# Performance work log

Hardware: AMD Instinct MI355X
Metric: run time of the kernel (lower is better)

Reference implementation:

```python
import jax, jax.numpy as jnp
import numpy as np

N = 100000   # nodes
E = 1600000  # edges
IN = 128
HID = 128    # 2 * out_channels
OUT = 64


def setup_inputs() -> dict:
    key = jax.random.key(0)
    ks = jax.random.split(key, 8)
    x = jax.random.normal(ks[0], (N, IN), dtype=jnp.float32)
    edge_index = jax.random.randint(ks[1], (2, E), 0, N, dtype=jnp.int32)
    s = 1.0 / np.sqrt(IN)
    W1 = jax.random.normal(ks[2], (IN, HID), dtype=jnp.float32) * s
    Wm1 = jax.random.normal(ks[3], (HID, HID), dtype=jnp.float32) * s
    Wm2 = jax.random.normal(ks[4], (HID, HID), dtype=jnp.float32) * s
    W2 = jax.random.normal(ks[5], (HID, OUT), dtype=jnp.float32) * s
    b1 = jnp.zeros((HID,), jnp.float32)
    bm1 = jnp.zeros((HID,), jnp.float32)
    bm2 = jnp.zeros((HID,), jnp.float32)
    b2 = jnp.zeros((OUT,), jnp.float32)
    return {"x": x, "edge_index": edge_index, "W1": W1, "b1": b1,
            "Wm1": Wm1, "bm1": bm1, "Wm2": Wm2, "bm2": bm2,
            "W2": W2, "b2": b2}


def _gcn_norm(edge_index, num_nodes):
    # PyG GCNConv: add self-loops (weight 1), symmetric normalization.
    loop = jnp.arange(num_nodes, dtype=edge_index.dtype)
    src = jnp.concatenate([edge_index[0], loop])
    dst = jnp.concatenate([edge_index[1], loop])
    deg = jax.ops.segment_sum(jnp.ones_like(src, jnp.float32), dst,
                              num_segments=num_nodes)
    dinv = jnp.where(deg > 0, jax.lax.rsqrt(deg), 0.0)
    norm = dinv[src] * dinv[dst]  # [E + N]
    return src, dst, norm


def _gcn_conv(h, W, b, src, dst, norm, num_nodes):
    h = h @ W                                # dense transform [N, F_out]
    msg = h[src] * norm[:, None]             # gather + scale   [E+N, F_out]
    out = jax.ops.segment_sum(msg, dst, num_segments=num_nodes)  # scatter-add
    return out + b


def reference(x, edge_index, W1, b1, Wm1, bm1, Wm2, bm2, W2, b2):
    num_nodes = x.shape[0]
    src, dst, norm = _gcn_norm(edge_index, num_nodes)
    h = jax.nn.relu(_gcn_conv(x, W1, b1, src, dst, norm, num_nodes))
    h = jax.nn.relu(_gcn_conv(h, Wm1, bm1, src, dst, norm, num_nodes))
    h = jax.nn.relu(_gcn_conv(h, Wm2, bm2, src, dst, norm, num_nodes))
    return _gcn_conv(h, W2, b2, src, dst, norm, num_nodes)  # [N, OUT]
```

## Files before the change

kernel.cpp:

```cpp
#include <hip/hip_runtime.h>
#include <hip/hip_bf16.h>
#include <hip/hip_fp16.h>


#define NNODES 100000
#define NEDGES 1600000

typedef __attribute__((ext_vector_type(8))) short bf16x8;
typedef __attribute__((ext_vector_type(4))) float f32x4;


__device__ inline float2 h2f2(unsigned int u) {
    __half2 h = *reinterpret_cast<__half2*>(&u);
    return __half22float2(h);
}
__device__ inline unsigned int f22h2(float a, float b) {
    __half2 h = __floats2half2_rn(a, b);
    return *reinterpret_cast<unsigned int*>(&h);
}

__device__ inline void split1(float x, short& hi, short& lo) {
    unsigned int u = __float_as_uint(x);
    hi = (short)(u >> 16);
    float r = x - __uint_as_float(u & 0xFFFF0000u);
    lo = (short)(__float_as_uint(r) >> 16);
}

__device__ inline void split8f(const float* f, bf16x8& hi, bf16x8& lo) {
#pragma unroll
    for (int i = 0; i < 8; i++) { short h, l; split1(f[i], h, l); hi[i] = h; lo[i] = l; }
}


__global__ void zero_ints(int* p, int n) {
    int i = blockIdx.x * blockDim.x + threadIdx.x;
    if (i < n) p[i] = 0;
}

__global__ void count_deg(const int* __restrict__ dst, int* __restrict__ deg, int e) {
    int i = blockIdx.x * blockDim.x + threadIdx.x;
    if (i < e) atomicAdd(&deg[dst[i]], 1);
}

__global__ void compute_dinv(const int* __restrict__ deg, float* __restrict__ dinv, int n) {
    int i = blockIdx.x * blockDim.x + threadIdx.x;
    if (i < n) dinv[i] = rsqrtf((float)(deg[i] + 1));
}

__global__ void scan_block_sums(const int* __restrict__ deg, int* __restrict__ bsum, int n) {
    __shared__ int sd[256];
    int t = threadIdx.x;
    int base = blockIdx.x * 1024 + t * 4;
    int s = 0;
#pragma unroll
    for (int j = 0; j < 4; j++) { int i = base + j; if (i < n) s += deg[i]; }
    sd[t] = s; __syncthreads();
    for (int off = 128; off > 0; off >>= 1) {
        if (t < off) sd[t] += sd[t + off];
        __syncthreads();
    }
    if (t == 0) bsum[blockIdx.x] = sd[0];
}

__global__ void scan_small_exclusive(int* __restrict__ bsum, int nb,
                                     int* __restrict__ row_ptr, int n, int e) {
    __shared__ int sd[256];
    int t = threadIdx.x;
    int v = (t < nb) ? bsum[t] : 0;
    sd[t] = v; __syncthreads();
    for (int off = 1; off < 256; off <<= 1) {
        int x = (t >= off) ? sd[t - off] : 0;
        __syncthreads();
        sd[t] += x;
        __syncthreads();
    }
    if (t < nb) bsum[t] = sd[t] - v;
    if (t == 0) row_ptr[n] = e;
}

__global__ void scan_write(const int* __restrict__ deg, const int* __restrict__ bsum,
                           int* __restrict__ row_ptr, int n) {
    __shared__ int sd[256];
    int t = threadIdx.x;
    int base = blockIdx.x * 1024 + t * 4;
    int v[4]; int s = 0;
#pragma unroll
    for (int j = 0; j < 4; j++) { int i = base + j; v[j] = (i < n) ? deg[i] : 0; s += v[j]; }
    sd[t] = s; __syncthreads();
    for (int off = 1; off < 256; off <<= 1) {
        int x = (t >= off) ? sd[t - off] : 0;
        __syncthreads();
        sd[t] += x;
        __syncthreads();
    }
    int run = bsum[blockIdx.x] + (sd[t] - s);
#pragma unroll
    for (int j = 0; j < 4; j++) {
        int i = base + j;
        if (i < n) row_ptr[i] = run;
        run += v[j];
    }
}

__global__ void fill_csr(const int* __restrict__ src, const int* __restrict__ dst,
                         const int* __restrict__ row_ptr, int* __restrict__ fill,
                         int* __restrict__ col, int e) {
    int i = blockIdx.x * blockDim.x + threadIdx.x;
    if (i < e) {
        int d = dst[i];
        int o = atomicAdd(&fill[d], 1);
        col[row_ptr[d] + o] = src[i];
    }
}


template <int N>
__global__ void conv_wfrag(const float* __restrict__ W, unsigned short* __restrict__ hi,
                           unsigned short* __restrict__ lo) {
    constexpr int NT = N / 16;
    int e = blockIdx.x * 256 + threadIdx.x;
    if (e >= 4 * NT * 64 * 8) return;
    int j = e & 7;
    int l = (e >> 3) & 63;
    int t = (e >> 9) % NT;
    int c = e / (512 * NT);
    int k = c * 32 + (l >> 4) * 8 + j;
    int n = t * 16 + (l & 15);
    float x = W[k * N + n];
    short h, lw; split1(x, h, lw);
    hi[e] = (unsigned short)h;
    lo[e] = (unsigned short)lw;
}


template <typename AT, int BN>
__global__ __launch_bounds__(256) void gemm_mfma(const AT* __restrict__ A,
                                                 const unsigned short* __restrict__ gwhi,
                                                 const unsigned short* __restrict__ gwlo,
                                                 const float* __restrict__ dinv,
                                                 __half* __restrict__ T, int nrows) {
    constexpr int NT = BN / 16;
    constexpr int WFRAG = 4 * NT * 64 * 8;
    __shared__ __align__(16) unsigned short s_hi[WFRAG];
    __shared__ __align__(16) unsigned short s_lo[WFRAG];
    int tid = threadIdx.x;
    for (int i = tid; i < WFRAG / 8; i += 256) {
        ((uint4*)s_hi)[i] = ((const uint4*)gwhi)[i];
        ((uint4*)s_lo)[i] = ((const uint4*)gwlo)[i];
    }
    __syncthreads();

    int wave = tid >> 6, lane = tid & 63;
    int m = lane & 15, q = lane >> 4;
    long row0 = ((long)blockIdx.x * 4 + wave) * 32;
    if (row0 >= nrows) return;
    long rowa = row0 + m;
    bool hasb = (row0 + 16) < nrows;
    long rowb = hasb ? (row0 + 16 + m) : rowa;

    f32x4 acc[2][NT];
#pragma unroll
    for (int s = 0; s < 2; s++)
#pragma unroll
        for (int t = 0; t < NT; t++)
#pragma unroll
            for (int r = 0; r < 4; r++) acc[s][t][r] = 0.f;

#pragma unroll
    for (int c = 0; c < 4; c++) {
        bf16x8 ah[2], al[2];
        float fa[8], fb[8];
        if constexpr (sizeof(AT) == 2) {
            uint4 ra = *(const uint4*)((const __half*)A + rowa * 128 + c * 32 + q * 8);
            uint4 rb = *(const uint4*)((const __half*)A + rowb * 128 + c * 32 + q * 8);
            float2 t0;
            t0 = h2f2(ra.x); fa[0] = t0.x; fa[1] = t0.y;
            t0 = h2f2(ra.y); fa[2] = t0.x; fa[3] = t0.y;
            t0 = h2f2(ra.z); fa[4] = t0.x; fa[5] = t0.y;
            t0 = h2f2(ra.w); fa[6] = t0.x; fa[7] = t0.y;
            t0 = h2f2(rb.x); fb[0] = t0.x; fb[1] = t0.y;
            t0 = h2f2(rb.y); fb[2] = t0.x; fb[3] = t0.y;
            t0 = h2f2(rb.z); fb[4] = t0.x; fb[5] = t0.y;
            t0 = h2f2(rb.w); fb[6] = t0.x; fb[7] = t0.y;
        } else {
            const float* pa = (const float*)A + rowa * 128 + c * 32 + q * 8;
            const float* pb = (const float*)A + rowb * 128 + c * 32 + q * 8;
            *(float4*)&fa[0] = *(const float4*)pa;
            *(float4*)&fa[4] = *(const float4*)(pa + 4);
            *(float4*)&fb[0] = *(const float4*)pb;
            *(float4*)&fb[4] = *(const float4*)(pb + 4);
        }
        split8f(fa, ah[0], al[0]);
        split8f(fb, ah[1], al[1]);

#pragma unroll
        for (int t = 0; t < NT; t++) {
            bf16x8 bhi = *(const bf16x8*)(s_hi + ((c * NT + t) * 64 + lane) * 8);
            bf16x8 blo = *(const bf16x8*)(s_lo + ((c * NT + t) * 64 + lane) * 8);
#pragma unroll
            for (int s = 0; s < 2; s++) {
                acc[s][t] = __builtin_amdgcn_mfma_f32_16x16x32_bf16(al[s], bhi, acc[s][t], 0, 0, 0);
                acc[s][t] = __builtin_amdgcn_mfma_f32_16x16x32_bf16(ah[s], blo, acc[s][t], 0, 0, 0);
                acc[s][t] = __builtin_amdgcn_mfma_f32_16x16x32_bf16(ah[s], bhi, acc[s][t], 0, 0, 0);
            }
        }
    }

#pragma unroll
    for (int s = 0; s < 2; s++) {
        if (s == 1 && !hasb) break;
#pragma unroll
        for (int r = 0; r < 4; r++) {
            long row = row0 + s * 16 + q * 4 + r;
            if (row < nrows) {
                float di = dinv[row];
#pragma unroll
                for (int t = 0; t < NT; t++)
                    T[row * BN + t * 16 + m] = __float2half(acc[s][t][r] * di);
            }
        }
    }
}


__device__ inline void acc8(float* a, uint4 v) {
    float2 f0 = h2f2(v.x), f1 = h2f2(v.y), f2 = h2f2(v.z), f3 = h2f2(v.w);
    a[0] += f0.x; a[1] += f0.y; a[2] += f1.x; a[3] += f1.y;
    a[4] += f2.x; a[5] += f2.y; a[6] += f3.x; a[7] += f3.y;
}
__device__ inline void acc4(float* a, uint2 v) {
    float2 f0 = h2f2(v.x), f1 = h2f2(v.y);
    a[0] += f0.x; a[1] += f0.y; a[2] += f1.x; a[3] += f1.y;
}

__global__ __launch_bounds__(256) void agg128h(const __half* __restrict__ t,
                                               const int* __restrict__ row_ptr,
                                               const int* __restrict__ col,
                                               const float* __restrict__ dinv,
                                               const float* __restrict__ bias,
                                               __half* __restrict__ out, int n) {
    int wave = threadIdx.x >> 6, lane = threadIdx.x & 63;
    int node = blockIdx.x * 4 + wave;
    if (node >= n) return;
    int q = lane >> 4, i = lane & 15;
    int r0 = row_ptr[node], r1 = row_ptr[node + 1];
    const uint4* t4 = (const uint4*)t;

    float a0[8], a1[8], a2[8], a3[8];
#pragma unroll
    for (int k = 0; k < 8; k++) { a0[k] = 0.f; a1[k] = 0.f; a2[k] = 0.f; a3[k] = 0.f; }

    int p = r0;
    for (; p + 16 <= r1; p += 16) {
        int c0 = col[p + q];
        int c1 = col[p + 4 + q];
        int c2 = col[p + 8 + q];
        int c3 = col[p + 12 + q];
        uint4 v0 = t4[(size_t)c0 * 16 + i];
        uint4 v1 = t4[(size_t)c1 * 16 + i];
        uint4 v2 = t4[(size_t)c2 * 16 + i];
        uint4 v3 = t4[(size_t)c3 * 16 + i];
        acc8(a0, v0); acc8(a1, v1); acc8(a2, v2); acc8(a3, v3);
    }
    for (; p + 8 <= r1; p += 8) {
        int c0 = col[p + q];
        int c1 = col[p + 4 + q];
        uint4 v0 = t4[(size_t)c0 * 16 + i];
        uint4 v1 = t4[(size_t)c1 * 16 + i];
        acc8(a0, v0); acc8(a1, v1);
    }
    for (; p < r1; p += 4) {
        int idx = p + q;
        if (idx < r1) {
            int c = col[idx];
            acc8(a0, t4[(size_t)c * 16 + i]);
        }
    }

    float s[8];
#pragma unroll
    for (int k = 0; k < 8; k++) s[k] = (a0[k] + a1[k]) + (a2[k] + a3[k]);
#pragma unroll
    for (int k = 0; k < 8; k++) s[k] += __shfl_xor(s[k], 16);
#pragma unroll
    for (int k = 0; k < 8; k++) s[k] += __shfl_xor(s[k], 32);

    if (q == 0) {
        uint4 ownv = t4[(size_t)node * 16 + i];
        float own[8];
        float2 f0 = h2f2(ownv.x), f1 = h2f2(ownv.y), f2 = h2f2(ownv.z), f3 = h2f2(ownv.w);
        own[0] = f0.x; own[1] = f0.y; own[2] = f1.x; own[3] = f1.y;
        own[4] = f2.x; own[5] = f2.y; own[6] = f3.x; own[7] = f3.y;
        float di = dinv[node];
        float4 bA = ((const float4*)bias)[i * 2];
        float4 bB = ((const float4*)bias)[i * 2 + 1];
        float o[8];
        o[0] = di * (s[0] + own[0]) + bA.x;
        o[1] = di * (s[1] + own[1]) + bA.y;
        o[2] = di * (s[2] + own[2]) + bA.z;
        o[3] = di * (s[3] + own[3]) + bA.w;
        o[4] = di * (s[4] + own[4]) + bB.x;
        o[5] = di * (s[5] + own[5]) + bB.y;
        o[6] = di * (s[6] + own[6]) + bB.z;
        o[7] = di * (s[7] + own[7]) + bB.w;
#pragma unroll
        for (int k = 0; k < 8; k++) o[k] = fmaxf(o[k], 0.f);
        uint4 ov;
        ov.x = f22h2(o[0], o[1]); ov.y = f22h2(o[2], o[3]);
        ov.z = f22h2(o[4], o[5]); ov.w = f22h2(o[6], o[7]);
        ((uint4*)out)[(size_t)node * 16 + i] = ov;
    }
}

__global__ __launch_bounds__(256) void agg64h(const __half* __restrict__ t,
                                              const int* __restrict__ row_ptr,
                                              const int* __restrict__ col,
                                              const float* __restrict__ dinv,
                                              const float* __restrict__ bias,
                                              float* __restrict__ out, int n) {
    int wave = threadIdx.x >> 6, lane = threadIdx.x & 63;
    int node = blockIdx.x * 4 + wave;
    if (node >= n) return;
    int q = lane >> 4, i = lane & 15;
    int r0 = row_ptr[node], r1 = row_ptr[node + 1];
    const uint2* t2 = (const uint2*)t;

    float a0[4], a1[4], a2[4], a3[4];
#pragma unroll
    for (int k = 0; k < 4; k++) { a0[k] = 0.f; a1[k] = 0.f; a2[k] = 0.f; a3[k] = 0.f; }

    int p = r0;
    for (; p + 16 <= r1; p += 16) {
        int c0 = col[p + q];
        int c1 = col[p + 4 + q];
        int c2 = col[p + 8 + q];
        int c3 = col[p + 12 + q];
        uint2 v0 = t2[(size_t)c0 * 16 + i];
        uint2 v1 = t2[(size_t)c1 * 16 + i];
        uint2 v2 = t2[(size_t)c2 * 16 + i];
        uint2 v3 = t2[(size_t)c3 * 16 + i];
        acc4(a0, v0); acc4(a1, v1); acc4(a2, v2); acc4(a3, v3);
    }
    for (; p + 8 <= r1; p += 8) {
        int c0 = col[p + q];
        int c1 = col[p + 4 + q];
        uint2 v0 = t2[(size_t)c0 * 16 + i];
        uint2 v1 = t2[(size_t)c1 * 16 + i];
        acc4(a0, v0); acc4(a1, v1);
    }
    for (; p < r1; p += 4) {
        int idx = p + q;
        if (idx < r1) {
            int c = col[idx];
            acc4(a0, t2[(size_t)c * 16 + i]);
        }
    }

    float s[4];
#pragma unroll
    for (int k = 0; k < 4; k++) s[k] = (a0[k] + a1[k]) + (a2[k] + a3[k]);
#pragma unroll
    for (int k = 0; k < 4; k++) s[k] += __shfl_xor(s[k], 16);
#pragma unroll
    for (int k = 0; k < 4; k++) s[k] += __shfl_xor(s[k], 32);

    if (q == 0) {
        uint2 ownv = t2[(size_t)node * 16 + i];
        float own[4];
        float2 f0 = h2f2(ownv.x), f1 = h2f2(ownv.y);
        own[0] = f0.x; own[1] = f0.y; own[2] = f1.x; own[3] = f1.y;
        float di = dinv[node];
        float4 b4 = ((const float4*)bias)[i];
        float4 o;
        o.x = di * (s[0] + own[0]) + b4.x;
        o.y = di * (s[1] + own[1]) + b4.y;
        o.z = di * (s[2] + own[2]) + b4.z;
        o.w = di * (s[3] + own[3]) + b4.w;
        ((float4*)out)[(size_t)node * 16 + i] = o;
    }
}


extern "C" void kernel_launch(void* const* d_in, const int* in_sizes, int n_in,
                              void* d_out, int out_size, void* d_ws, size_t ws_size,
                              hipStream_t stream) {
    const int N = NNODES, E = NEDGES;
    const float* x   = (const float*)d_in[0];
    const int*   ei  = (const int*)d_in[1];
    const int*   src = ei;
    const int*   dst = ei + E;
    const float* W1  = (const float*)d_in[2];
    const float* b1  = (const float*)d_in[3];
    const float* Wm1 = (const float*)d_in[4];
    const float* bm1 = (const float*)d_in[5];
    const float* Wm2 = (const float*)d_in[6];
    const float* bm2 = (const float*)d_in[7];
    const float* W2  = (const float*)d_in[8];
    const float* b2  = (const float*)d_in[9];
    float* out = (float*)d_out;

    int* deg     = (int*)d_ws;
    int* fill    = deg + N;
    int* row_ptr = fill + N;
    int* bsum    = row_ptr + (N + 4);
    int* col     = bsum + 256;
    float* dinv  = (float*)(col + E);
    __half* t16  = (__half*)(dinv + N);
    __half* bufA = t16 + (size_t)N * 128;
    unsigned short* whi1  = (unsigned short*)(bufA + (size_t)N * 128);
    unsigned short* wlo1  = whi1 + 16384;
    unsigned short* whiM1 = wlo1 + 16384;
    unsigned short* wloM1 = whiM1 + 16384;
    unsigned short* whiM2 = wloM1 + 16384;
    unsigned short* wloM2 = whiM2 + 16384;
    unsigned short* whi2  = wloM2 + 16384;
    unsigned short* wlo2  = whi2 + 8192;

    const int NBLK = (N + 1023) / 1024;
    const int EB   = (E + 255) / 256;

    zero_ints<<<(2 * N + 255) / 256, 256, 0, stream>>>(deg, 2 * N);
    count_deg<<<EB, 256, 0, stream>>>(dst, deg, E);
    compute_dinv<<<(N + 255) / 256, 256, 0, stream>>>(deg, dinv, N);
    scan_block_sums<<<NBLK, 256, 0, stream>>>(deg, bsum, N);
    scan_small_exclusive<<<1, 256, 0, stream>>>(bsum, NBLK, row_ptr, N, E);
    scan_write<<<NBLK, 256, 0, stream>>>(deg, bsum, row_ptr, N);
    fill_csr<<<EB, 256, 0, stream>>>(src, dst, row_ptr, fill, col, E);

    conv_wfrag<128><<<64, 256, 0, stream>>>(W1, whi1, wlo1);
    conv_wfrag<128><<<64, 256, 0, stream>>>(Wm1, whiM1, wloM1);
    conv_wfrag<128><<<64, 256, 0, stream>>>(Wm2, whiM2, wloM2);
    conv_wfrag<64><<<32, 256, 0, stream>>>(W2, whi2, wlo2);

    const int GB = (N + 127) / 128;
    const int AB = (N + 3) / 4;

    gemm_mfma<float, 128><<<GB, 256, 0, stream>>>(x, whi1, wlo1, dinv, t16, N);
    agg128h<<<AB, 256, 0, stream>>>(t16, row_ptr, col, dinv, b1, bufA, N);

    gemm_mfma<__half, 128><<<GB, 256, 0, stream>>>(bufA, whiM1, wloM1, dinv, t16, N);
    agg128h<<<AB, 256, 0, stream>>>(t16, row_ptr, col, dinv, bm1, bufA, N);

    gemm_mfma<__half, 128><<<GB, 256, 0, stream>>>(bufA, whiM2, wloM2, dinv, t16, N);
    agg128h<<<AB, 256, 0, stream>>>(t16, row_ptr, col, dinv, bm2, bufA, N);

    gemm_mfma<__half, 64><<<GB, 256, 0, stream>>>(bufA, whi2, wlo2, dinv, t16, N);
    agg64h<<<AB, 256, 0, stream>>>(t16, row_ptr, col, dinv, b2, out, N);
}
```

Baseline: 656.0 us.

## Build CSR via two-level bucket sort with shared-memory histograms

Replaces the global-atomic degree count, multi-kernel scan and per-edge atomic CSR fill with a bucketed counting sort. Edges are first histogrammed into 782 buckets of 128 destination nodes in shared memory, then scattered into bucket-contiguous packed entries, then each bucket block builds its local row_ptr, dinv and col with shared-memory atomics. The four weight-fragment conversion kernels are also merged into one launch. This cuts global atomic contention and launch count, at the cost of an extra packed edge buffer and a second pass over dst.

```diff
diff --git a/kernel.cpp b/kernel.cpp
--- a/kernel.cpp
+++ b/kernel.cpp
@@ -5,6 +5,7 @@
 
 #define NNODES 100000
 #define NEDGES 1600000
+#define NBUCK 782
 
 typedef __attribute__((ext_vector_type(8))) short bf16x8;
 typedef __attribute__((ext_vector_type(4))) float f32x4;
@@ -37,55 +38,35 @@
     if (i < n) p[i] = 0;
 }
 
-__global__ void count_deg(const int* __restrict__ dst, int* __restrict__ deg, int e) {
-    int i = blockIdx.x * blockDim.x + threadIdx.x;
-    if (i < e) atomicAdd(&deg[dst[i]], 1);
-}
-
-__global__ void compute_dinv(const int* __restrict__ deg, float* __restrict__ dinv, int n) {
-    int i = blockIdx.x * blockDim.x + threadIdx.x;
-    if (i < n) dinv[i] = rsqrtf((float)(deg[i] + 1));
-}
-
-__global__ void scan_block_sums(const int* __restrict__ deg, int* __restrict__ bsum, int n) {
+__global__ __launch_bounds__(256) void hist_pass(const int* __restrict__ dst,
+                                                 int* __restrict__ cnt, int e) {
+    __shared__ int h[NBUCK];
+    int tid = threadIdx.x;
+    for (int i = tid; i < NBUCK; i += 256) h[i] = 0;
+    __syncthreads();
+    int base_e = blockIdx.x * 4096;
+#pragma unroll
+    for (int j = 0; j < 16; j++) {
+        int i = base_e + j * 256 + tid;
+        if (i < e) atomicAdd(&h[dst[i] >> 7], 1);
+    }
+    __syncthreads();
+    for (int b = tid; b < NBUCK; b += 256)
+        if (h[b]) atomicAdd(&cnt[b], h[b]);
+}
+
+__global__ __launch_bounds__(256) void scan_buckets(const int* __restrict__ cnt,
+                                                    int* __restrict__ base,
+                                                    int* __restrict__ fill, int e) {
     __shared__ int sd[256];
     int t = threadIdx.x;
-    int base = blockIdx.x * 1024 + t * 4;
-    int s = 0;
-#pragma unroll
-    for (int j = 0; j < 4; j++) { int i = base + j; if (i < n) s += deg[i]; }
-    sd[t] = s; __syncthreads();
-    for (int off = 128; off > 0; off >>= 1) {
-        if (t < off) sd[t] += sd[t + off];
-        __syncthreads();
-    }
-    if (t == 0) bsum[blockIdx.x] = sd[0];
-}
-
-__global__ void scan_small_exclusive(int* __restrict__ bsum, int nb,
-                                     int* __restrict__ row_ptr, int n, int e) {
-    __shared__ int sd[256];
-    int t = threadIdx.x;
-    int v = (t < nb) ? bsum[t] : 0;
-    sd[t] = v; __syncthreads();
-    for (int off = 1; off < 256; off <<= 1) {
-        int x = (t >= off) ? sd[t - off] : 0;
-        __syncthreads();
-        sd[t] += x;
-        __syncthreads();
-    }
-    if (t < nb) bsum[t] = sd[t] - v;
-    if (t == 0) row_ptr[n] = e;
-}
-
-__global__ void scan_write(const int* __restrict__ deg, const int* __restrict__ bsum,
-                           int* __restrict__ row_ptr, int n) {
-    __shared__ int sd[256];
-    int t = threadIdx.x;
-    int base = blockIdx.x * 1024 + t * 4;
     int v[4]; int s = 0;
 #pragma unroll
-    for (int j = 0; j < 4; j++) { int i = base + j; v[j] = (i < n) ? deg[i] : 0; s += v[j]; }
+    for (int j = 0; j < 4; j++) {
+        int i = t * 4 + j;
+        v[j] = (i < NBUCK) ? cnt[i] : 0;
+        s += v[j];
+    }
     sd[t] = s; __syncthreads();
     for (int off = 1; off < 256; off <<= 1) {
         int x = (t >= off) ? sd[t - off] : 0;
@@ -93,43 +74,113 @@
         sd[t] += x;
         __syncthreads();
     }
-    int run = bsum[blockIdx.x] + (sd[t] - s);
+    int run = sd[t] - s;
 #pragma unroll
     for (int j = 0; j < 4; j++) {
-        int i = base + j;
-        if (i < n) row_ptr[i] = run;
+        int i = t * 4 + j;
+        if (i < NBUCK) { base[i] = run; fill[i] = run; }
         run += v[j];
     }
-}
-
-__global__ void fill_csr(const int* __restrict__ src, const int* __restrict__ dst,
-                         const int* __restrict__ row_ptr, int* __restrict__ fill,
-                         int* __restrict__ col, int e) {
-    int i = blockIdx.x * blockDim.x + threadIdx.x;
-    if (i < e) {
-        int d = dst[i];
-        int o = atomicAdd(&fill[d], 1);
-        col[row_ptr[d] + o] = src[i];
-    }
-}
-
-
-template <int N>
-__global__ void conv_wfrag(const float* __restrict__ W, unsigned short* __restrict__ hi,
-                           unsigned short* __restrict__ lo) {
-    constexpr int NT = N / 16;
-    int e = blockIdx.x * 256 + threadIdx.x;
-    if (e >= 4 * NT * 64 * 8) return;
+    if (t == 0) base[NBUCK] = e;
+}
+
+__global__ __launch_bounds__(256) void scatter_pass(const int* __restrict__ src,
+                                                    const int* __restrict__ dst,
+                                                    int* __restrict__ fill,
+                                                    unsigned int* __restrict__ epart, int e) {
+    __shared__ int h[NBUCK];
+    int tid = threadIdx.x;
+    for (int i = tid; i < NBUCK; i += 256) h[i] = 0;
+    __syncthreads();
+    int base_e = blockIdx.x * 4096;
+#pragma unroll
+    for (int j = 0; j < 16; j++) {
+        int i = base_e + j * 256 + tid;
+        if (i < e) atomicAdd(&h[dst[i] >> 7], 1);
+    }
+    __syncthreads();
+    for (int b = tid; b < NBUCK; b += 256)
+        if (h[b]) h[b] = atomicAdd(&fill[b], h[b]);
+    __syncthreads();
+#pragma unroll
+    for (int j = 0; j < 16; j++) {
+        int i = base_e + j * 256 + tid;
+        if (i < e) {
+            int d = dst[i];
+            int bk = d >> 7;
+            int pos = atomicAdd(&h[bk], 1);
+            epart[pos] = ((unsigned int)src[i] << 7) | (unsigned int)(d & 127);
+        }
+    }
+}
+
+__global__ __launch_bounds__(256) void build_csr(const unsigned int* __restrict__ epart,
+                                                 const int* __restrict__ base,
+                                                 int* __restrict__ row_ptr,
+                                                 int* __restrict__ col,
+                                                 float* __restrict__ dinv,
+                                                 int n, int e_total) {
+    __shared__ int deg[128], off[128], fil[128];
+    int b = blockIdx.x, tid = threadIdx.x;
+    int node0 = b << 7;
+    int nn = n - node0; if (nn > 128) nn = 128;
+    int e0 = base[b], e1 = base[b + 1];
+    int cnt = e1 - e0;
+
+    if (tid < 128) deg[tid] = 0;
+    __syncthreads();
+    for (int i = tid; i < cnt; i += 256)
+        atomicAdd(&deg[epart[e0 + i] & 127], 1);
+    __syncthreads();
+    if (tid < 128) off[tid] = deg[tid];
+    __syncthreads();
+    for (int o = 1; o < 128; o <<= 1) {
+        int x = (tid < 128 && tid >= o) ? off[tid - o] : 0;
+        __syncthreads();
+        if (tid < 128) off[tid] += x;
+        __syncthreads();
+    }
+    if (tid < nn) {
+        int ex = e0 + off[tid] - deg[tid];
+        row_ptr[node0 + tid] = ex;
+        fil[tid] = ex;
+        dinv[node0 + tid] = rsqrtf((float)(deg[tid] + 1));
+    }
+    if (b == 0 && tid == 0) row_ptr[n] = e_total;
+    __syncthreads();
+    for (int i = tid; i < cnt; i += 256) {
+        unsigned int u = epart[e0 + i];
+        int ld = (int)(u & 127);
+        int pos = atomicAdd(&fil[ld], 1);
+        col[pos] = (int)(u >> 7);
+    }
+}
+
+
+__device__ inline void wfrag_one(const float* W, unsigned short* hi, unsigned short* lo,
+                                 int e, int NT, int Ncols) {
     int j = e & 7;
     int l = (e >> 3) & 63;
     int t = (e >> 9) % NT;
     int c = e / (512 * NT);
     int k = c * 32 + (l >> 4) * 8 + j;
     int n = t * 16 + (l & 15);
-    float x = W[k * N + n];
+    float x = W[k * Ncols + n];
     short h, lw; split1(x, h, lw);
     hi[e] = (unsigned short)h;
     lo[e] = (unsigned short)lw;
+}
+
+__global__ void conv_all(const float* W1, unsigned short* hi1, unsigned short* lo1,
+                         const float* Wm1, unsigned short* him1, unsigned short* lom1,
+                         const float* Wm2, unsigned short* him2, unsigned short* lom2,
+                         const float* W2, unsigned short* hi2, unsigned short* lo2) {
+    int blk = blockIdx.x;
+    int tid = threadIdx.x;
+    if (blk < 64)        wfrag_one(W1,  hi1,  lo1,  blk * 256 + tid,        8, 128);
+    else if (blk < 128)  wfrag_one(Wm1, him1, lom1, (blk - 64) * 256 + tid, 8, 128);
+    else if (blk < 192)  wfrag_one(Wm2, him2, lom2, (blk - 128) * 256 + tid, 8, 128);
+    else                 wfrag_one(W2,  hi2,  lo2,  (blk - 192) * 256 + tid, 4, 64);
 }
 
 
@@ -399,12 +450,13 @@
     const float* b2  = (const float*)d_in[9];
     float* out = (float*)d_out;
 
-    int* deg     = (int*)d_ws;
-    int* fill    = deg + N;
-    int* row_ptr = fill + N;
-    int* bsum    = row_ptr + (N + 4);
-    int* col     = bsum + 256;
-    float* dinv  = (float*)(col + E);
+    int* bucket_cnt  = (int*)d_ws;
+    int* bucket_base = bucket_cnt + 784;
+    int* bucket_fill = bucket_base + 784;
+    int* row_ptr     = bucket_fill + 784;
+    int* col         = row_ptr + (N + 4);
+    unsigned int* epart = (unsigned int*)(col + E);
+    float* dinv  = (float*)(epart + E);
     __half* t16  = (__half*)(dinv + N);
     __half* bufA = t16 + (size_t)N * 128;
     unsigned short* whi1  = (unsigned short*)(bufA + (size_t)N * 128);
@@ -416,21 +468,16 @@
     unsigned short* whi2  = wloM2 + 16384;
     unsigned short* wlo2  = whi2 + 8192;
 
-    const int NBLK = (N + 1023) / 1024;
-    const int EB   = (E + 255) / 256;
-
-    zero_ints<<<(2 * N + 255) / 256, 256, 0, stream>>>(deg, 2 * N);
-    count_deg<<<EB, 256, 0, stream>>>(dst, deg, E);
-    compute_dinv<<<(N + 255) / 256, 256, 0, stream>>>(deg, dinv, N);
-    scan_block_sums<<<NBLK, 256, 0, stream>>>(deg, bsum, N);
-    scan_small_exclusive<<<1, 256, 0, stream>>>(bsum, NBLK, row_ptr, N, E);
-    scan_write<<<NBLK, 256, 0, stream>>>(deg, bsum, row_ptr, N);
-    fill_csr<<<EB, 256, 0, stream>>>(src, dst, row_ptr, fill, col, E);
-
-    conv_wfrag<128><<<64, 256, 0, stream>>>(W1, whi1, wlo1);
-    conv_wfrag<128><<<64, 256, 0, stream>>>(Wm1, whiM1, wloM1);
-    conv_wfrag<128><<<64, 256, 0, stream>>>(Wm2, whiM2, wloM2);
-    conv_wfrag<64><<<32, 256, 0, stream>>>(W2, whi2, wlo2);
+    const int EB4 = (E + 4095) / 4096;
+
+    zero_ints<<<4, 256, 0, stream>>>(bucket_cnt, NBUCK);
+    hist_pass<<<EB4, 256, 0, stream>>>(dst, bucket_cnt, E);
+    scan_buckets<<<1, 256, 0, stream>>>(bucket_cnt, bucket_base, bucket_fill, E);
+    scatter_pass<<<EB4, 256, 0, stream>>>(src, dst, bucket_fill, epart, E);
+    build_csr<<<NBUCK, 256, 0, stream>>>(epart, bucket_base, row_ptr, col, dinv, N, E);
+
+    conv_all<<<224, 256, 0, stream>>>(W1, whi1, wlo1, Wm1, whiM1, wloM1,
+                                      Wm2, whiM2, wloM2, W2, whi2, wlo2);
 
     const int GB = (N + 127) / 128;
     const int AB = (N + 3) / 4;
```

Measured after the change: 557.3 us. 1.18x faster.
